# Kernel tuning notes

Hardware: AMD Instinct MI355X
Metric: run time of the kernel (lower is better)

## Reference

```python
import jax, jax.numpy as jnp
import numpy as np

B, N, D, P = 32, 16, 64, 8  # batch, num_objs, in_feat_dim, patch size
PAIRS = N * (N - 1)


def _conv_relu(x, W, b):
    # Conv2d(kernel=3, stride=1, padding=1) + ReLU, NCHW/OIHW layout
    y = jax.lax.conv_general_dilated(
        x, W, window_strides=(1, 1), padding='SAME',
        dimension_numbers=('NCHW', 'OIHW', 'NCHW'))
    return jax.nn.relu(y + b[None, :, None, None])


def setup_inputs() -> dict:
    key = jax.random.key(0)
    ks = jax.random.split(key, 12)
    x = jax.random.normal(ks[0], (B, N, D, P, P), jnp.float32)
    # g_idx: cols 0,1 index into the repeated pair axis of size N*(N-1); col 2 is a 0/1 mask
    i0 = jax.random.randint(ks[1], (B, PAIRS, 1), 0, PAIRS)
    i1 = jax.random.randint(ks[2], (B, PAIRS, 1), 0, PAIRS)
    m = jax.random.randint(ks[3], (B, PAIRS, 1), 0, 2)
    g_idx = jnp.concatenate([i0, i1, m], axis=2)

    def w(k, o, i):
        return jax.random.normal(k, (o, i, 3, 3), jnp.float32) * (1.0 / np.sqrt(i * 9.0))

    return {
        'x': x, 'g_idx': g_idx,
        'W_rel': w(ks[4], D, 2 * D), 'b_rel': jnp.zeros((D,), jnp.float32),
        'W_self': w(ks[5], D, D), 'b_self': jnp.zeros((D,), jnp.float32),
        'W_aff': w(ks[6], D, D), 'b_aff': jnp.zeros((D,), jnp.float32),
        'W_agg': w(ks[7], D, 2 * D), 'b_agg': jnp.zeros((D,), jnp.float32),
    }


def reference(x, g_idx, W_rel, b_rel, W_self, b_self, W_aff, b_aff, W_agg, b_agg):
    b, n, d, p, _ = x.shape
    pairs = n * (n - 1)
    s = x
    # x1: [B, N*(N-1), D, P, P]
    x1 = jnp.tile(x, (1, n - 1, 1, 1, 1))

    def gather_pair(col):
        idx = g_idx[:, :, col][:, :, None, None, None]  # [B, pairs, 1, 1, 1]
        idx = jnp.broadcast_to(idx, (b, pairs, d, p, p))
        return jnp.take_along_axis(x1, idx, axis=1)

    y1 = gather_pair(0)
    y2 = gather_pair(1)
    mask = g_idx[:, :, 2][:, :, None, None, None].astype(x.dtype)
    r = jnp.concatenate([y1, y2], axis=2) * mask  # [B, pairs, 2D, P, P]
    r = _conv_relu(r.reshape(-1, 2 * d, p, p), W_rel, b_rel)
    r = r.reshape(b, n, n - 1, d, p, p).sum(axis=2)  # scatter-sum per object

    xs = _conv_relu(x.reshape(-1, d, p, p), W_self, b_self).reshape(b, n, d, p, p)
    pred = xs + r
    a = _conv_relu(pred.reshape(-1, d, p, p), W_aff, b_aff).reshape(b, n, d, p, p)
    a = jnp.concatenate([a, s], axis=2)  # [B, N, 2D, P, P]
    out = _conv_relu(a.reshape(-1, 2 * d, p, p), W_agg, b_agg).reshape(b, n, d, p, p)
    return out
```

## Files before the change

kernel.cpp:

```cpp
#include <hip/hip_runtime.h>


#define NIMG 512
#define IMGSZ 4096

using bf16x8 = __attribute__((ext_vector_type(8))) short;
using f32x4  = __attribute__((ext_vector_type(4))) float;

__device__ inline unsigned short f2bf(float f) {
  union { float f; unsigned u; } v; v.f = f;
  unsigned r = v.u + 0x7fffu + ((v.u >> 16) & 1u);
  return (unsigned short)(r >> 16);
}

__device__ inline f32x4 bf4_to_f32(uint2 p) {
  union { unsigned u; float f; } c;
  f32x4 r;
  c.u = (p.x & 0xffffu) << 16;  r[0] = c.f;
  c.u = (p.x & 0xffff0000u);    r[1] = c.f;
  c.u = (p.y & 0xffffu) << 16;  r[2] = c.f;
  c.u = (p.y & 0xffff0000u);    r[3] = c.f;
  return r;
}

__global__ __launch_bounds__(256) void prep_w(
    const float* __restrict__ Wr, const float* __restrict__ Ws,
    const float* __restrict__ Wa, const float* __restrict__ Wg,
    unsigned short* __restrict__ Wt)
{
  int idx = blockIdx.x * 256 + threadIdx.x;
  if (idx >= 221184) return;
  float v;
  if (idx < 73728) {
    int c = idx / 36864, r = idx % 36864;
    int t = r >> 12, oc = (r >> 6) & 63, ic = r & 63;
    v = (c == 0 ? Ws : Wa)[oc * 576 + ic * 9 + t];
  } else {
    int r2 = idx - 73728;
    int half = r2 / 73728, rr = r2 % 73728;
    int t = rr >> 13, oc = (rr >> 7) & 63, ic = rr & 127;
    v = (half ? Wg : Wr)[oc * 1152 + ic * 9 + t];
  }
  Wt[idx] = f2bf(v);
}

__device__ inline void decode_img(int j, int& b, int& o) {
  b = ((j >> 7) << 3) | (j & 7);
  o = (j >> 3) & 15;
}

template<int ROWX>
__device__ inline void stage_x(const float* __restrict__ xb,
                               unsigned short* __restrict__ s,
                               int coff, int w, int px) {
#pragma unroll
  for (int r = 0; r < 8; ++r) {
    int ic0 = (w + 4 * r) * 2;
    const float* sp = xb + ic0 * 64;
    float a = sp[px], c = sp[64 + px];
    *(unsigned*)(s + px * ROWX + coff + ic0) =
        (unsigned)f2bf(a) | ((unsigned)f2bf(c) << 16);
  }
}

__global__ __launch_bounds__(256) void k1(
    const float* __restrict__ x,
    const unsigned short* __restrict__ Wt,
    unsigned short* __restrict__ cA, unsigned short* __restrict__ cB)
{
  constexpr int ROW = 72;
  __shared__ __align__(16) unsigned short sX[65 * ROW];
  int b, o;
  decode_img(blockIdx.x, b, o);
  const int img = b * 16 + o;
  const int tid = threadIdx.x;
  const int w = tid >> 6, lane = tid & 63;

  stage_x<ROW>(x + (size_t)img * IMGSZ, sX, 0, w, lane);
  if (tid < 36) ((unsigned*)(sX + 64 * ROW))[tid] = 0;
  __syncthreads();

  const int q = lane >> 4, n16 = lane & 15;
  const int ocb = w * 16;
  const int co = ocb + q * 4;

  int pyt[4], pxt[4];
#pragma unroll
  for (int t = 0; t < 4; ++t) { int p = t * 16 + n16; pyt[t] = p >> 3; pxt[t] = p & 7; }

  f32x4 aA[4] = {}, aB[4] = {};
  const unsigned short* WA = Wt + 73728 + (ocb + n16) * 128 + q * 8;
  const unsigned short* WB = WA + 64;
#pragma unroll
  for (int tap = 0; tap < 9; ++tap) {
    const int dy = tap / 3 - 1, dx = tap % 3 - 1;
    int spt[4];
#pragma unroll
    for (int t = 0; t < 4; ++t) {
      int sy = pyt[t] + dy, sx = pxt[t] + dx;
      spt[t] = ((unsigned)sy < 8u && (unsigned)sx < 8u) ? (sy * 8 + sx) : 64;
    }
#pragma unroll
    for (int ks = 0; ks < 2; ++ks) {
      bf16x8 aa = *(const bf16x8*)(WA + tap * 8192 + ks * 32);
      bf16x8 ab = *(const bf16x8*)(WB + tap * 8192 + ks * 32);
#pragma unroll
      for (int t = 0; t < 4; ++t) {
        bf16x8 bt = *(const bf16x8*)(sX + spt[t] * ROW + ks * 32 + q * 8);
        aA[t] = __builtin_amdgcn_mfma_f32_16x16x32_bf16(aa, bt, aA[t], 0, 0, 0);
        aB[t] = __builtin_amdgcn_mfma_f32_16x16x32_bf16(ab, bt, aB[t], 0, 0, 0);
      }
    }
  }

  const size_t ib = (size_t)img * IMGSZ;
#pragma unroll
  for (int t = 0; t < 4; ++t) {
    int p = t * 16 + n16;
    uint2 pa, pb;
    pa.x = (unsigned)f2bf(aA[t][0]) | ((unsigned)f2bf(aA[t][1]) << 16);
    pa.y = (unsigned)f2bf(aA[t][2]) | ((unsigned)f2bf(aA[t][3]) << 16);
    pb.x = (unsigned)f2bf(aB[t][0]) | ((unsigned)f2bf(aB[t][1]) << 16);
    pb.y = (unsigned)f2bf(aB[t][2]) | ((unsigned)f2bf(aB[t][3]) << 16);
    *(uint2*)(cA + ib + p * 64 + co) = pa;
    *(uint2*)(cB + ib + p * 64 + co) = pb;
  }
}

__global__ __launch_bounds__(256, 2) void k2(
    const float* __restrict__ x,
    const int* __restrict__ g_idx,
    const unsigned short* __restrict__ Wt,
    const float* __restrict__ b_rel, const float* __restrict__ b_self,
    const float* __restrict__ b_aff, const float* __restrict__ b_agg,
    const unsigned short* __restrict__ cA, const unsigned short* __restrict__ cB,
    float* __restrict__ out)
{
  constexpr int ROW = 72, ROW2 = 136, XROW = 68;
  __shared__ __align__(16) unsigned short sX[65 * ROW2];
  __shared__ __align__(16) unsigned short sPred[65 * ROW];
  __shared__ __align__(16) float sXS[64 * XROW];
  __shared__ int so1a[16], so2a[16];
  __shared__ float sma[16];
  __shared__ int s_na;

  int b, i;
  decode_img(blockIdx.x, b, i);
  const int img = b * 16 + i;
  const int tid = threadIdx.x;
  const int w = tid >> 6, lane = tid & 63;

  int o1v = 0, o2v = 0, mv = 0;
  if (tid < 15) {
    const int* gp = g_idx + ((size_t)b * 240 + i * 15 + tid) * 3;
    o1v = gp[0] & 15;
    o2v = gp[1] & 15;
    mv  = gp[2];
  }
  if (tid < 64) {
    if (tid < 16) { so1a[tid] = 0; so2a[tid] = 0; sma[tid] = 0.f; }
    unsigned long long mk = __ballot(mv != 0);
    int pfx = (int)__popcll(mk & ((1ull << tid) - 1));
    if (mv) { so1a[pfx] = o1v; so2a[pfx] = o2v; sma[pfx] = 1.f; }
    if (tid == 0) s_na = (int)__popcll(mk);
  }

  stage_x<ROW2>(x + (size_t)img * IMGSZ, sX, 64, w, lane);
  if (tid < 68) ((unsigned*)(sX + 64 * ROW2))[tid] = 0;
  if (tid < 36) ((unsigned*)(sPred + 64 * ROW))[tid] = 0;
  __syncthreads();

  const int q = lane >> 4, n16 = lane & 15;
  const int ocb = w * 16;
  const int co = ocb + q * 4;
  const int aw64  = (ocb + n16) * 64 + q * 8;
  const int aw128 = (ocb + n16) * 128 + q * 8;

  int pyt[4], pxt[4];
#pragma unroll
  for (int t = 0; t < 4; ++t) { int p = t * 16 + n16; pyt[t] = p >> 3; pxt[t] = p & 7; }

  {
    f32x4 f[4] = {};
    const unsigned short* WS = Wt + aw64;
#pragma unroll
    for (int tap = 0; tap < 9; ++tap) {
      const int dy = tap / 3 - 1, dx = tap % 3 - 1;
      int spt[4];
#pragma unroll
      for (int t = 0; t < 4; ++t) {
        int sy = pyt[t] + dy, sx = pxt[t] + dx;
        spt[t] = ((unsigned)sy < 8u && (unsigned)sx < 8u) ? (sy * 8 + sx) : 64;
      }
#pragma unroll
      for (int ks = 0; ks < 2; ++ks) {
        bf16x8 a = *(const bf16x8*)(WS + tap * 4096 + ks * 32);
#pragma unroll
        for (int t = 0; t < 4; ++t) {
          bf16x8 bt = *(const bf16x8*)(sX + spt[t] * ROW2 + 64 + ks * 32 + q * 8);
          f[t] = __builtin_amdgcn_mfma_f32_16x16x32_bf16(a, bt, f[t], 0, 0, 0);
        }
      }
    }
#pragma unroll
    for (int t = 0; t < 4; ++t) {
      int p = t * 16 + n16;
      f32x4 vs = f[t];
#pragma unroll
      for (int r = 0; r < 4; ++r) vs[r] = fmaxf(vs[r] + b_self[co + r], 0.f);
      *(f32x4*)(sXS + p * XROW + co) = vs;
    }
  }
  __syncthreads();

  {
    const size_t bb = (size_t)b * 16 * IMGSZ;
    const int na = s_na;
    const int nc = (na + 3) >> 2;
    const float c0 = (float)(15 - na);
#pragma unroll 1
    for (int pass = 0; pass < 4; ++pass) {
      const int e = tid * 4 + pass * 1024;
      const int e_px = e >> 6, e_ic = e & 63;
      f32x4 xv = *(const f32x4*)(sXS + e_px * XROW + e_ic);
      float acc[4], br[4];
#pragma unroll
      for (int r = 0; r < 4; ++r) {
        br[r] = b_rel[e_ic + r];
        acc[r] = xv[r] + c0 * fmaxf(br[r], 0.f);
      }
#pragma unroll 1
      for (int c = 0; c < nc; ++c) {
        uint2 v1[4], v2[4];
#pragma unroll
        for (int jj = 0; jj < 4; ++jj) {
          int j = c * 4 + jj;
          v1[jj] = *(const uint2*)(cA + bb + (size_t)so1a[j] * IMGSZ + e);
          v2[jj] = *(const uint2*)(cB + bb + (size_t)so2a[j] * IMGSZ + e);
        }
#pragma unroll
        for (int jj = 0; jj < 4; ++jj) {
          float s = sma[c * 4 + jj];
          f32x4 a1 = bf4_to_f32(v1[jj]);
          f32x4 a2 = bf4_to_f32(v2[jj]);
#pragma unroll
          for (int r = 0; r < 4; ++r)
            acc[r] += s * fmaxf(a1[r] + a2[r] + br[r], 0.f);
        }
      }
      uint2 pk;
      pk.x = (unsigned)f2bf(acc[0]) | ((unsigned)f2bf(acc[1]) << 16);
      pk.y = (unsigned)f2bf(acc[2]) | ((unsigned)f2bf(acc[3]) << 16);
      *(uint2*)(sPred + e_px * ROW + e_ic) = pk;
    }
  }
  __syncthreads();

  {
    f32x4 f[4] = {};
    const unsigned short* WA = Wt + 36864 + aw64;
#pragma unroll
    for (int tap = 0; tap < 9; ++tap) {
      const int dy = tap / 3 - 1, dx = tap % 3 - 1;
      int spt[4];
#pragma unroll
      for (int t = 0; t < 4; ++t) {
        int sy = pyt[t] + dy, sx = pxt[t] + dx;
        spt[t] = ((unsigned)sy < 8u && (unsigned)sx < 8u) ? (sy * 8 + sx) : 64;
      }
#pragma unroll
      for (int ks = 0; ks < 2; ++ks) {
        bf16x8 a = *(const bf16x8*)(WA + tap * 4096 + ks * 32);
#pragma unroll
        for (int t = 0; t < 4; ++t) {
          bf16x8 bt = *(const bf16x8*)(sPred + spt[t] * ROW + ks * 32 + q * 8);
          f[t] = __builtin_amdgcn_mfma_f32_16x16x32_bf16(a, bt, f[t], 0, 0, 0);
        }
      }
    }
#pragma unroll
    for (int t = 0; t < 4; ++t) {
      int p = t * 16 + n16;
      float v0 = fmaxf(f[t][0] + b_aff[co + 0], 0.f);
      float v1 = fmaxf(f[t][1] + b_aff[co + 1], 0.f);
      float v2 = fmaxf(f[t][2] + b_aff[co + 2], 0.f);
      float v3 = fmaxf(f[t][3] + b_aff[co + 3], 0.f);
      uint2 pk;
      pk.x = (unsigned)f2bf(v0) | ((unsigned)f2bf(v1) << 16);
      pk.y = (unsigned)f2bf(v2) | ((unsigned)f2bf(v3) << 16);
      *(uint2*)(sX + p * ROW2 + co) = pk;
    }
  }
  __syncthreads();

  {
    f32x4 g[4] = {};
    const unsigned short* WG = Wt + 147456 + aw128;
#pragma unroll
    for (int tap = 0; tap < 9; ++tap) {
      const int dy = tap / 3 - 1, dx = tap % 3 - 1;
      int spt[4];
#pragma unroll
      for (int t = 0; t < 4; ++t) {
        int sy = pyt[t] + dy, sx = pxt[t] + dx;
        spt[t] = ((unsigned)sy < 8u && (unsigned)sx < 8u) ? (sy * 8 + sx) : 64;
      }
#pragma unroll
      for (int ks = 0; ks < 4; ++ks) {
        bf16x8 a = *(const bf16x8*)(WG + tap * 8192 + ks * 32);
#pragma unroll
        for (int t = 0; t < 4; ++t) {
          bf16x8 bt = *(const bf16x8*)(sX + spt[t] * ROW2 + ks * 32 + q * 8);
          g[t] = __builtin_amdgcn_mfma_f32_16x16x32_bf16(bt, a, g[t], 0, 0, 0);
        }
      }
    }
    float* ob = out + (size_t)img * IMGSZ;
    const float bg = b_agg[ocb + n16];
#pragma unroll
    for (int t = 0; t < 4; ++t) {
      f32x4 v;
#pragma unroll
      for (int r = 0; r < 4; ++r) v[r] = fmaxf(g[t][r] + bg, 0.f);
      *(f32x4*)(ob + (ocb + n16) * 64 + t * 16 + q * 4) = v;
    }
  }
}

extern "C" void kernel_launch(void* const* d_in, const int* in_sizes, int n_in,
                              void* d_out, int out_size, void* d_ws, size_t ws_size,
                              hipStream_t stream) {
  const float* x      = (const float*)d_in[0];
  const int*   g_idx  = (const int*)  d_in[1];
  const float* W_rel  = (const float*)d_in[2];
  const float* b_rel  = (const float*)d_in[3];
  const float* W_self = (const float*)d_in[4];
  const float* b_self = (const float*)d_in[5];
  const float* W_aff  = (const float*)d_in[6];
  const float* b_aff  = (const float*)d_in[7];
  const float* W_agg  = (const float*)d_in[8];
  const float* b_agg  = (const float*)d_in[9];
  float* out = (float*)d_out;

  unsigned short* cA = (unsigned short*)d_ws;
  unsigned short* cB = cA + 2097152;
  unsigned short* Wt = cB + 2097152;

  prep_w<<<864, 256, 0, stream>>>(W_rel, W_self, W_aff, W_agg, Wt);
  k1<<<NIMG, 256, 0, stream>>>(x, Wt, cA, cB);
  k2<<<NIMG, 256, 0, stream>>>(x, g_idx, Wt, b_rel, b_self, b_aff, b_agg,
                               cA, cB, out);
}
```

Measured before the change: 117.4 us.

## Use 512-thread blocks for k1/k2 and vectorize weight prep stores

Both main kernels now launch 512 threads per block. In k1 the two halves of the block each compute one of the two relation-conv partial outputs (cA or cB), so each wave holds one set of accumulators instead of two. In k2 the extra waves share the input staging and the gather/relu/sum phase, while the convolutions run on only the first 256 threads. The weight-prep kernel now converts four elements per thread with one packed store. This aims to raise memory-level parallelism and occupancy, but it leaves half the waves idle during the k2 conv phases and puts more register and LDS pressure on each block.

```diff
diff --git a/kernel.cpp b/kernel.cpp
--- a/kernel.cpp
+++ b/kernel.cpp
@@ -28,20 +28,29 @@
     const float* __restrict__ Wa, const float* __restrict__ Wg,
     unsigned short* __restrict__ Wt)
 {
-  int idx = blockIdx.x * 256 + threadIdx.x;
-  if (idx >= 221184) return;
-  float v;
-  if (idx < 73728) {
-    int c = idx / 36864, r = idx % 36864;
-    int t = r >> 12, oc = (r >> 6) & 63, ic = r & 63;
-    v = (c == 0 ? Ws : Wa)[oc * 576 + ic * 9 + t];
-  } else {
-    int r2 = idx - 73728;
-    int half = r2 / 73728, rr = r2 % 73728;
-    int t = rr >> 13, oc = (rr >> 7) & 63, ic = rr & 127;
-    v = (half ? Wg : Wr)[oc * 1152 + ic * 9 + t];
-  }
-  Wt[idx] = f2bf(v);
+  int i4 = (blockIdx.x * 256 + threadIdx.x) * 4;
+  if (i4 >= 221184) return;
+  unsigned short o4[4];
+#pragma unroll
+  for (int e = 0; e < 4; ++e) {
+    int idx = i4 + e;
+    float v;
+    if (idx < 73728) {
+      int c = idx / 36864, r = idx % 36864;
+      int t = r >> 12, oc = (r >> 6) & 63, ic = r & 63;
+      v = (c == 0 ? Ws : Wa)[oc * 576 + ic * 9 + t];
+    } else {
+      int r2 = idx - 73728;
+      int half = r2 / 73728, rr = r2 % 73728;
+      int t = rr >> 13, oc = (rr >> 7) & 63, ic = rr & 127;
+      v = (half ? Wg : Wr)[oc * 1152 + ic * 9 + t];
+    }
+    o4[e] = f2bf(v);
+  }
+  uint2 pk;
+  pk.x = (unsigned)o4[0] | ((unsigned)o4[1] << 16);
+  pk.y = (unsigned)o4[2] | ((unsigned)o4[3] << 16);
+  *(uint2*)(Wt + i4) = pk;
 }
 
 __device__ inline void decode_img(int j, int& b, int& o) {
@@ -50,12 +59,12 @@
 }
 
 template<int ROWX>
-__device__ inline void stage_x(const float* __restrict__ xb,
-                               unsigned short* __restrict__ s,
-                               int coff, int w, int px) {
-#pragma unroll
-  for (int r = 0; r < 8; ++r) {
-    int ic0 = (w + 4 * r) * 2;
+__device__ inline void stage_x512(const float* __restrict__ xb,
+                                  unsigned short* __restrict__ s,
+                                  int coff, int w8, int px) {
+#pragma unroll
+  for (int r = 0; r < 4; ++r) {
+    int ic0 = (w8 + 8 * r) * 2;
     const float* sp = xb + ic0 * 64;
     float a = sp[px], c = sp[64 + px];
     *(unsigned*)(s + px * ROWX + coff + ic0) =
@@ -63,7 +72,7 @@
   }
 }
 
-__global__ __launch_bounds__(256) void k1(
+__global__ __launch_bounds__(512, 4) void k1(
     const float* __restrict__ x,
     const unsigned short* __restrict__ Wt,
     unsigned short* __restrict__ cA, unsigned short* __restrict__ cB)
@@ -74,12 +83,14 @@
   decode_img(blockIdx.x, b, o);
   const int img = b * 16 + o;
   const int tid = threadIdx.x;
-  const int w = tid >> 6, lane = tid & 63;
-
-  stage_x<ROW>(x + (size_t)img * IMGSZ, sX, 0, w, lane);
+  const int w8 = tid >> 6, lane = tid & 63;
+
+  stage_x512<ROW>(x + (size_t)img * IMGSZ, sX, 0, w8, lane);
   if (tid < 36) ((unsigned*)(sX + 64 * ROW))[tid] = 0;
   __syncthreads();
 
+  const int half = tid >> 8;
+  const int w = w8 & 3;
   const int q = lane >> 4, n16 = lane & 15;
   const int ocb = w * 16;
   const int co = ocb + q * 4;
@@ -88,9 +99,8 @@
 #pragma unroll
   for (int t = 0; t < 4; ++t) { int p = t * 16 + n16; pyt[t] = p >> 3; pxt[t] = p & 7; }
 
-  f32x4 aA[4] = {}, aB[4] = {};
-  const unsigned short* WA = Wt + 73728 + (ocb + n16) * 128 + q * 8;
-  const unsigned short* WB = WA + 64;
+  f32x4 acc[4] = {};
+  const unsigned short* WH = Wt + 73728 + (ocb + n16) * 128 + q * 8 + half * 64;
 #pragma unroll
   for (int tap = 0; tap < 9; ++tap) {
     const int dy = tap / 3 - 1, dx = tap % 3 - 1;
@@ -102,32 +112,28 @@
     }
 #pragma unroll
     for (int ks = 0; ks < 2; ++ks) {
-      bf16x8 aa = *(const bf16x8*)(WA + tap * 8192 + ks * 32);
-      bf16x8 ab = *(const bf16x8*)(WB + tap * 8192 + ks * 32);
+      bf16x8 aa = *(const bf16x8*)(WH + tap * 8192 + ks * 32);
 #pragma unroll
       for (int t = 0; t < 4; ++t) {
         bf16x8 bt = *(const bf16x8*)(sX + spt[t] * ROW + ks * 32 + q * 8);
-        aA[t] = __builtin_amdgcn_mfma_f32_16x16x32_bf16(aa, bt, aA[t], 0, 0, 0);
-        aB[t] = __builtin_amdgcn_mfma_f32_16x16x32_bf16(ab, bt, aB[t], 0, 0, 0);
-      }
-    }
-  }
-
+        acc[t] = __builtin_amdgcn_mfma_f32_16x16x32_bf16(aa, bt, acc[t], 0, 0, 0);
+      }
+    }
+  }
+
+  unsigned short* dst = half ? cB : cA;
   const size_t ib = (size_t)img * IMGSZ;
 #pragma unroll
   for (int t = 0; t < 4; ++t) {
     int p = t * 16 + n16;
-    uint2 pa, pb;
-    pa.x = (unsigned)f2bf(aA[t][0]) | ((unsigned)f2bf(aA[t][1]) << 16);
-    pa.y = (unsigned)f2bf(aA[t][2]) | ((unsigned)f2bf(aA[t][3]) << 16);
-    pb.x = (unsigned)f2bf(aB[t][0]) | ((unsigned)f2bf(aB[t][1]) << 16);
-    pb.y = (unsigned)f2bf(aB[t][2]) | ((unsigned)f2bf(aB[t][3]) << 16);
-    *(uint2*)(cA + ib + p * 64 + co) = pa;
-    *(uint2*)(cB + ib + p * 64 + co) = pb;
-  }
-}
-
-__global__ __launch_bounds__(256, 2) void k2(
+    uint2 pa;
+    pa.x = (unsigned)f2bf(acc[t][0]) | ((unsigned)f2bf(acc[t][1]) << 16);
+    pa.y = (unsigned)f2bf(acc[t][2]) | ((unsigned)f2bf(acc[t][3]) << 16);
+    *(uint2*)(dst + ib + p * 64 + co) = pa;
+  }
+}
+
+__global__ __launch_bounds__(512, 4) void k2(
     const float* __restrict__ x,
     const int* __restrict__ g_idx,
     const unsigned short* __restrict__ Wt,
@@ -148,7 +154,7 @@
   decode_img(blockIdx.x, b, i);
   const int img = b * 16 + i;
   const int tid = threadIdx.x;
-  const int w = tid >> 6, lane = tid & 63;
+  const int w8 = tid >> 6, lane = tid & 63;
 
   int o1v = 0, o2v = 0, mv = 0;
   if (tid < 15) {
@@ -165,11 +171,12 @@
     if (tid == 0) s_na = (int)__popcll(mk);
   }
 
-  stage_x<ROW2>(x + (size_t)img * IMGSZ, sX, 64, w, lane);
+  stage_x512<ROW2>(x + (size_t)img * IMGSZ, sX, 64, w8, lane);
   if (tid < 68) ((unsigned*)(sX + 64 * ROW2))[tid] = 0;
   if (tid < 36) ((unsigned*)(sPred + 64 * ROW))[tid] = 0;
   __syncthreads();
 
+  const int w = w8 & 3;
   const int q = lane >> 4, n16 = lane & 15;
   const int ocb = w * 16;
   const int co = ocb + q * 4;
@@ -180,7 +187,7 @@
 #pragma unroll
   for (int t = 0; t < 4; ++t) { int p = t * 16 + n16; pyt[t] = p >> 3; pxt[t] = p & 7; }
 
-  {
+  if (tid < 256) {
     f32x4 f[4] = {};
     const unsigned short* WS = Wt + aw64;
 #pragma unroll
@@ -219,8 +226,8 @@
     const int nc = (na + 3) >> 2;
     const float c0 = (float)(15 - na);
 #pragma unroll 1
-    for (int pass = 0; pass < 4; ++pass) {
-      const int e = tid * 4 + pass * 1024;
+    for (int pass = 0; pass < 2; ++pass) {
+      const int e = tid * 4 + pass * 2048;
       const int e_px = e >> 6, e_ic = e & 63;
       f32x4 xv = *(const f32x4*)(sXS + e_px * XROW + e_ic);
       float acc[4], br[4];
@@ -256,7 +263,7 @@
   }
   __syncthreads();
 
-  {
+  if (tid < 256) {
     f32x4 f[4] = {};
     const unsigned short* WA = Wt + 36864 + aw64;
 #pragma unroll
@@ -293,7 +300,7 @@
   }
   __syncthreads();
 
-  {
+  if (tid < 256) {
     f32x4 g[4] = {};
     const unsigned short* WG = Wt + 147456 + aw128;
 #pragma unroll
@@ -346,8 +353,8 @@
   unsigned short* cB = cA + 2097152;
   unsigned short* Wt = cB + 2097152;
 
-  prep_w<<<864, 256, 0, stream>>>(W_rel, W_self, W_aff, W_agg, Wt);
-  k1<<<NIMG, 256, 0, stream>>>(x, Wt, cA, cB);
-  k2<<<NIMG, 256, 0, stream>>>(x, g_idx, Wt, b_rel, b_self, b_aff, b_agg,
+  prep_w<<<216, 256, 0, stream>>>(W_rel, W_self, W_aff, W_agg, Wt);
+  k1<<<NIMG, 512, 0, stream>>>(x, Wt, cA, cB);
+  k2<<<NIMG, 512, 0, stream>>>(x, g_idx, Wt, b_rel, b_self, b_aff, b_agg,
                                cA, cB, out);
 }
```

Measured after the change: 116.2 us, median of 2. About the same (-1.0%).
